# Performance work log

Measured on AMD Instinct MI355X. Metric: run time of the kernel, lower is better.

## Reference

```python
import jax, jax.numpy as jnp
import numpy as np

NUM_HEADS = 16
NEG_INF = float('-inf')


def setup_inputs() -> dict:
    key = jax.random.key(0)
    ks = jax.random.split(key, 8)
    B, S, D = 2, 2048, 1024
    return {
        "query": jax.random.normal(ks[0], (B, S, D), jnp.float32),
        "key": jax.random.normal(ks[1], (B, S, D), jnp.float32),
        "value": jax.random.normal(ks[2], (B, S, D), jnp.float32),
        "attention_mask": jnp.zeros((B, S, S), dtype=bool),
        "Wq": jax.random.normal(ks[3], (D, D), jnp.float32) * (D ** -0.5),
        "Wk": jax.random.normal(ks[4], (D, D), jnp.float32) * (D ** -0.5),
        "Wv": jax.random.normal(ks[5], (D, D), jnp.float32) * (D ** -0.5),
        "Wout": jax.random.normal(ks[6], (D, D), jnp.float32) * (D ** -0.5),
        "b_out": jnp.zeros((D,), jnp.float32),
        "is_causal": 1,
    }


def reference(query, key, value, attention_mask, Wq, Wk, Wv, Wout, b_out, is_causal):
    B, q_len, D = query.shape
    k_len = key.shape[1]
    H = NUM_HEADS
    dk = D // H
    # projections (torch Linear: x @ W.T), split heads -> [B, H, S, dk]
    q = (query @ Wq.T).reshape(B, q_len, H, dk).transpose(0, 2, 1, 3)
    k = (key @ Wk.T).reshape(B, k_len, H, dk).transpose(0, 2, 1, 3)
    v = (value @ Wv.T).reshape(B, k_len, H, dk).transpose(0, 2, 1, 3)
    scores = jnp.einsum('bhqd,bhkd->bhqk', q, k) / jnp.sqrt(jnp.float32(dk))
    if is_causal:
        causal = jnp.triu(jnp.ones((q_len, k_len), dtype=bool), k=1)
        scores = jnp.where(causal, NEG_INF, scores)
    # attn_mask True -> masked out; broadcast over heads
    scores = jnp.where(attention_mask[:, None, :, :], NEG_INF, scores)
    attn = jax.nn.softmax(scores, axis=-1)
    attn = jnp.where(jnp.isnan(attn), 0.0, attn)  # fully-masked rows -> 0
    out = jnp.einsum('bhqk,bhkd->bhqd', attn, v)
    out = out.transpose(0, 2, 1, 3).reshape(B, q_len, D)
    return out @ Wout.T + b_out
```

## Files before the change

kernel.cpp:

```cpp
#include <hip/hip_runtime.h>
#include <hip/hip_bf16.h>

typedef __attribute__((ext_vector_type(8))) short bf16x8;
typedef __attribute__((ext_vector_type(4))) float f32x4;
typedef unsigned long long u64;
typedef unsigned int u32;

#define MFMA(a,b,c) __builtin_amdgcn_mfma_f32_16x16x32_bf16(a,b,c,0,0,0)
#define NEG_INF (-__builtin_inff())
#define SCALE2 0.1803368801111244f

__device__ __forceinline__ unsigned short f2b(float f) {
  unsigned int u = __float_as_uint(f);
  u = u + 0x7fffu + ((u >> 16) & 1u);
  return (unsigned short)(u >> 16);
}

__device__ __forceinline__ u32 pkbf(float lo, float hi) {
  __hip_bfloat162 h = __float22bfloat162_rn(float2{lo, hi});
  return *reinterpret_cast<u32*>(&h);
}

__device__ __forceinline__ void gload_lds16(const unsigned short* g, unsigned short* l) {
  __builtin_amdgcn_global_load_lds((const __attribute__((address_space(1))) void*)g,
                                   (__attribute__((address_space(3))) void*)l, 16, 0, 0);
}

__global__ void cvt7(const float* s0, const float* s1, const float* s2,
                     const float* s3, const float* s4, const float* s5, const float* s6,
                     unsigned short* d0, unsigned short* d1, unsigned short* d2,
                     unsigned short* d3, unsigned short* d4, unsigned short* d5, unsigned short* d6,
                     int nbig, int nsmall) {
  const float* s; unsigned short* d; int n4;
  switch (blockIdx.y) {
    case 0: s=s0; d=d0; n4=nbig; break;
    case 1: s=s1; d=d1; n4=nbig; break;
    case 2: s=s2; d=d2; n4=nbig; break;
    case 3: s=s3; d=d3; n4=nsmall; break;
    case 4: s=s4; d=d4; n4=nsmall; break;
    case 5: s=s5; d=d5; n4=nsmall; break;
    default: s=s6; d=d6; n4=nsmall; break;
  }
  int i = blockIdx.x * blockDim.x + threadIdx.x;
  if (i < n4) {
    float4 v = reinterpret_cast<const float4*>(s)[i];
    ushort4 o;
    o.x = f2b(v.x); o.y = f2b(v.y); o.z = f2b(v.z); o.w = f2b(v.w);
    reinterpret_cast<ushort4*>(d)[i] = o;
  }
}

__global__ void pack_mask(const unsigned char* __restrict__ am, u64* __restrict__ pm, int nU) {
  int lane = threadIdx.x & 63;
  int wid = blockIdx.x * (blockDim.x >> 6) + (threadIdx.x >> 6);
  int stride = gridDim.x * (blockDim.x >> 6);
  for (int u = wid; u < nU; u += stride) {
    unsigned char v = am[(size_t)u * 64 + lane];
    u64 m = __ballot(v != 0);
    if (lane == 0) pm[u] = m;
  }
}

__global__ void mask_summary(const u64* __restrict__ pm, u32* __restrict__ ms, int rows, int nkt) {
  int lane = threadIdx.x & 63;
  int wid = (blockIdx.x * blockDim.x + threadIdx.x) >> 6;
  int nw = (gridDim.x * blockDim.x) >> 6;
  for (int rp = wid; rp < (rows >> 1); rp += nw) {
    int row = rp * 2 + (lane >> 5);
    int t = lane & 31;
    u64 v = pm[(size_t)row * nkt + t];
    u64 bm = __ballot(v != 0ULL);
    if (lane == 0)  ms[rp*2]     = (u32)bm;
    if (lane == 32) ms[rp*2 + 1] = (u32)(bm >> 32);
  }
}

__global__ __launch_bounds__(256) void qkv128s(
    const unsigned short* __restrict__ A,
    const unsigned short* __restrict__ Bw,
    unsigned short* __restrict__ Cqk,
    unsigned short* __restrict__ Cv)
{
  const int K = 1024;
  __shared__ unsigned short As[128*32];
  __shared__ unsigned short Bs[128*32];
  const int tid  = threadIdx.x;
  const int w    = tid >> 6, lane = tid & 63;
  const int wr   = w >> 1,   wc   = w & 1;
  const int g    = lane >> 4, li  = lane & 15;
  const int m0   = blockIdx.x * 128, n0 = blockIdx.y * 128;
  const int bq0  = (m0 >> 12) * 1024 + n0;

  f32x4 acc[4][4] = {};

  const int rS0 = (w*2+0)*16 + (lane>>2);
  const int rS1 = (w*2+1)*16 + (lane>>2);
  const int cS  = (lane&3)*8;
  const unsigned short* gA0 = A  + (size_t)(m0+rS0)*K + cS;
  const unsigned short* gA1 = A  + (size_t)(m0+rS1)*K + cS;
  const unsigned short* gB0 = Bw + (size_t)(bq0+rS0)*K + cS;
  const unsigned short* gB1 = Bw + (size_t)(bq0+rS1)*K + cS;
  unsigned short* lA0 = &As[(w*2+0)*512];
  unsigned short* lA1 = &As[(w*2+1)*512];
  unsigned short* lB0 = &Bs[(w*2+0)*512];
  unsigned short* lB1 = &Bs[(w*2+1)*512];

  for (int k0 = 0; k0 < K; k0 += 32) {
    gload_lds16(gA0 + k0, lA0);
    gload_lds16(gA1 + k0, lA1);
    gload_lds16(gB0 + k0, lB0);
    gload_lds16(gB1 + k0, lB1);
    __syncthreads();

    bf16x8 af[4], bf[4];
    #pragma unroll
    for (int i = 0; i < 4; ++i)
      af[i] = *(const bf16x8*)(&As[(wr*64 + i*16 + li)*32 + g*8]);
    #pragma unroll
    for (int j = 0; j < 4; ++j)
      bf[j] = *(const bf16x8*)(&Bs[(wc*64 + j*16 + li)*32 + g*8]);
    #pragma unroll
    for (int i = 0; i < 4; ++i)
      #pragma unroll
      for (int j = 0; j < 4; ++j)
        acc[i][j] = MFMA(af[i], bf[j], acc[i][j]);
    __syncthreads();
  }

  #pragma unroll
  for (int i = 0; i < 4; ++i) {
    #pragma unroll
    for (int j = 0; j < 4; ++j) {
      int col = n0 + wc*64 + j*16 + li;
      #pragma unroll
      for (int r = 0; r < 4; ++r) {
        int row = m0 + wr*64 + i*16 + g*4 + r;
        float v = acc[i][j][r];
        if (row < 8192) {
          size_t addr = (((size_t)(row >> 11) * 16 + (col >> 6)) * 2048 + (row & 2047)) * 64 + (col & 63);
          Cqk[addr] = f2b(v);
        } else {
          int tk = row & 4095;
          size_t addr = (((size_t)(tk >> 11) * 16 + (col >> 6)) * 64 + (col & 63)) * 2048 + (tk & 2047);
          Cv[addr] = f2b(v);
        }
      }
    }
  }
}

__global__ __launch_bounds__(256) void gemm64x64(
    const unsigned short* __restrict__ A,
    const unsigned short* __restrict__ Bw,
    float* __restrict__ Cf,
    const float* __restrict__ bias,
    int M, int N, int K)
{
  const int NT = 32;
  __shared__ unsigned short As[2][64*32];
  __shared__ unsigned short Bs[2][64*32];
  const int tid  = threadIdx.x;
  const int w    = tid >> 6, lane = tid & 63;
  const int wr   = w >> 1,   wc   = w & 1;
  const int g    = lane >> 4, li  = lane & 15;
  const int m0   = blockIdx.x * 64, n0 = blockIdx.y * 64;

  f32x4 acc[2][2] = {};
  const int crow = lane >> 2, ccol = (lane & 3) * 8;
  const unsigned short* gA = A  + (size_t)(m0 + w*16 + crow)*K + ccol;
  const unsigned short* gB = Bw + (size_t)(n0 + w*16 + crow)*K + ccol;

  gload_lds16(gA, &As[0][w*512]);
  gload_lds16(gB, &Bs[0][w*512]);
  __syncthreads();

  for (int t = 0; t < NT; ++t) {
    const int cur = t & 1;
    if (t + 1 < NT) {
      const int k1 = (t + 1) * 32;
      gload_lds16(gA + k1, &As[cur^1][w*512]);
      gload_lds16(gB + k1, &Bs[cur^1][w*512]);
    }
    bf16x8 af[2], bf[2];
    #pragma unroll
    for (int i = 0; i < 2; ++i)
      af[i] = *(const bf16x8*)(&As[cur][(wr*32 + i*16 + li)*32 + g*8]);
    #pragma unroll
    for (int j = 0; j < 2; ++j)
      bf[j] = *(const bf16x8*)(&Bs[cur][(wc*32 + j*16 + li)*32 + g*8]);
    #pragma unroll
    for (int i = 0; i < 2; ++i)
      #pragma unroll
      for (int j = 0; j < 2; ++j)
        acc[i][j] = MFMA(af[i], bf[j], acc[i][j]);
    __syncthreads();
  }

  #pragma unroll
  for (int i = 0; i < 2; ++i) {
    #pragma unroll
    for (int j = 0; j < 2; ++j) {
      int col = n0 + wc*32 + j*16 + li;
      #pragma unroll
      for (int r = 0; r < 4; ++r) {
        int row = m0 + wr*32 + i*16 + g*4 + r;
        Cf[(size_t)row*N + col] = acc[i][j][r] + bias[col];
      }
    }
  }
}

__global__ __launch_bounds__(256, 4) void attn_kernel(
    const unsigned short* __restrict__ Qh,
    const unsigned short* __restrict__ Kh,
    const unsigned short* __restrict__ Vt,
    const u64* __restrict__ pmask,
    const u32* __restrict__ msum,
    const int* __restrict__ causal_p,
    unsigned short* __restrict__ Ob,
    int B, int H, int S)
{
  __shared__ unsigned short Ks [64*64];
  __shared__ unsigned short Vts[64*64];

  const int tid = threadIdx.x, w = tid >> 6, lane = tid & 63;
  const int g = lane >> 4, li = lane & 15;
  const int nkt = S >> 6, nqt = S >> 6;
  const int causal = causal_p[0];

  int id = blockIdx.x;
  int par = (id ^ (id >> 8)) & 1;
  int qh  = ((id >> 1) & 15) ^ (((id >> 8) & 3) << 2);
  int bh  = id >> 5;
  int qt  = par ? (nqt - 1 - qh) : qh;
  const int q0 = qt << 6;
  const int b = bh / H, h = bh % H;
  const size_t baseK = (size_t)bh * S * 64;
  const size_t baseV = (size_t)bh * 64 * S;

  const int qg = q0 + w*16 + li;
  const unsigned short* qp = Qh + baseK + (size_t)qg*64 + g*8;
  const bf16x8 qf0 = *(const bf16x8*)(qp);
  const bf16x8 qf1 = *(const bf16x8*)(qp + 32);

  const u32 sOr = msum[(size_t)b*S + qg];

  f32x4 oacc[4] = {};
  float mrun = -1e30f, lrun = 0.f;

  const int colk  = (lane & 7) ^ ((lane >> 3) & 7);
  const int ldrow = lane >> 3;
  const int ntile = causal ? (qt + 1) : nkt;

  for (int t = 0; t < ntile; ++t) {
    const int kv0 = t << 6;
    __syncthreads();
    #pragma unroll
    for (int s2 = 0; s2 < 2; ++s2) {
      int u = w*2 + s2;
      gload_lds16(Kh + baseK + (size_t)(kv0 + u*8 + ldrow)*64 + colk*8, &Ks[u*512]);
      gload_lds16(Vt + baseV + (size_t)(u*8 + ldrow)*S + kv0 + colk*8, &Vts[u*512]);
    }
    __syncthreads();

    f32x4 sa[4];
    #pragma unroll
    for (int ni = 0; ni < 4; ++ni) sa[ni] = (f32x4){0.f, 0.f, 0.f, 0.f};
    #pragma unroll
    for (int ni = 0; ni < 4; ++ni) {
      int row = ni*16 + li, rx = row & 7;
      bf16x8 k0 = *(const bf16x8*)(&Ks[row*64 + ((g     ^ rx))*8]);
      bf16x8 k1 = *(const bf16x8*)(&Ks[row*64 + (((4+g) ^ rx))*8]);
      sa[ni] = MFMA(k0, qf0, sa[ni]);
      sa[ni] = MFMA(k1, qf1, sa[ni]);
    }

    const bool edge   = (causal != 0) && (t == ntile - 1);
    const bool doMask = __any(((sOr >> t) & 1u) != 0u);
    float corr = 1.0f;
    bool rescale = true;

    if (!edge && !doMask) {
      float pe[4][4];
      #pragma unroll
      for (int ni = 0; ni < 4; ++ni)
        #pragma unroll
        for (int r = 0; r < 4; ++r)
          pe[ni][r] = exp2f(fmaf(sa[ni][r], SCALE2, -mrun));
      float a0 = fmaxf(sa[0][0], sa[0][1]), a1 = fmaxf(sa[0][2], sa[0][3]);
      float a2 = fmaxf(sa[1][0], sa[1][1]), a3 = fmaxf(sa[1][2], sa[1][3]);
      float a4 = fmaxf(sa[2][0], sa[2][1]), a5 = fmaxf(sa[2][2], sa[2][3]);
      float a6 = fmaxf(sa[3][0], sa[3][1]), a7 = fmaxf(sa[3][2], sa[3][3]);
      float mx = fmaxf(fmaxf(fmaxf(a0,a1), fmaxf(a2,a3)),
                       fmaxf(fmaxf(a4,a5), fmaxf(a6,a7)));
      mx = fmaxf(mx, __shfl_xor(mx, 16));
      mx = fmaxf(mx, __shfl_xor(mx, 32));
      float mxs = mx * SCALE2;
      if (__all(mxs <= mrun + 8.0f)) {
        float s0 = (pe[0][0]+pe[0][1]) + (pe[0][2]+pe[0][3]);
        float s1 = (pe[1][0]+pe[1][1]) + (pe[1][2]+pe[1][3]);
        float s2 = (pe[2][0]+pe[2][1]) + (pe[2][2]+pe[2][3]);
        float s3 = (pe[3][0]+pe[3][1]) + (pe[3][2]+pe[3][3]);
        float rs = (s0+s1) + (s2+s3);
        rs += __shfl_xor(rs, 16);
        rs += __shfl_xor(rs, 32);
        lrun += rs;
        #pragma unroll
        for (int ni = 0; ni < 4; ++ni)
          #pragma unroll
          for (int r = 0; r < 4; ++r)
            sa[ni][r] = pe[ni][r];
        rescale = false;
      } else {
        float mu = fmaxf(mrun, mxs);
        corr = exp2f(mrun - mu);
        float rs = 0.f;
        #pragma unroll
        for (int ni = 0; ni < 4; ++ni)
          #pragma unroll
          for (int r = 0; r < 4; ++r) {
            float p = exp2f(fmaf(sa[ni][r], SCALE2, -mu));
            sa[ni][r] = p;
            rs += p;
          }
        rs += __shfl_xor(rs, 16);
        rs += __shfl_xor(rs, 32);
        lrun = lrun * corr + rs;
        mrun = mu;
      }
    } else {
      u64 mrow = doMask ? pmask[((size_t)b*S + qg) * nkt + t] : 0ULL;
      #pragma unroll
      for (int ni = 0; ni < 4; ++ni)
        #pragma unroll
        for (int r = 0; r < 4; ++r) {
          int kvloc = ni*16 + g*4 + r;
          bool dead = (edge && (kv0 + kvloc > qg)) || ((mrow >> kvloc) & 1ULL);
          sa[ni][r] = dead ? NEG_INF : sa[ni][r] * SCALE2;
        }
      float mx = sa[0][0];
      #pragma unroll
      for (int ni = 0; ni < 4; ++ni)
        #pragma unroll
        for (int r = 0; r < 4; ++r)
          if (ni + r) mx = fmaxf(mx, sa[ni][r]);
      mx = fmaxf(mx, __shfl_xor(mx, 16));
      mx = fmaxf(mx, __shfl_xor(mx, 32));
      float mu = fmaxf(mrun, mx);
      corr = exp2f(mrun - mu);
      float rs = 0.f;
      #pragma unroll
      for (int ni = 0; ni < 4; ++ni)
        #pragma unroll
        for (int r = 0; r < 4; ++r) {
          float pe = exp2f(sa[ni][r] - mu);
          sa[ni][r] = pe;
          rs += pe;
        }
      rs += __shfl_xor(rs, 16);
      rs += __shfl_xor(rs, 32);
      lrun = lrun * corr + rs;
      mrun = mu;
    }

    bf16x8 pf[2];
    #pragma unroll
    for (int c = 0; c < 2; ++c) {
      u32 PA0 = pkbf(sa[2*c  ][0], sa[2*c  ][1]);
      u32 PA1 = pkbf(sa[2*c  ][2], sa[2*c  ][3]);
      u32 PB0 = pkbf(sa[2*c+1][0], sa[2*c+1][1]);
      u32 PB1 = pkbf(sa[2*c+1][2], sa[2*c+1][3]);
      u32 X16_0 = (u32)__shfl_xor((int)((g==2) ? PB0 : PA0), 16);
      u32 X16_1 = (u32)__shfl_xor((int)((g==2) ? PB1 : PA1), 16);
      u32 X32_0 = (u32)__shfl_xor((int)((g==0) ? PB0 : PA0), 32);
      u32 X32_1 = (u32)__shfl_xor((int)((g==0) ? PB1 : PA1), 32);
      u32 X48_0 = (u32)__shfl_xor((int)((g==1) ? PB0 : PA0), 48);
      u32 X48_1 = (u32)__shfl_xor((int)((g==1) ? PB1 : PA1), 48);
      union { u32 u[4]; bf16x8 v; } pbu;
      pbu.u[0] = (g==0) ? PA0   : (g==1) ? X48_0 : (g==2) ? X32_0 : X16_0;
      pbu.u[1] = (g==0) ? PA1   : (g==1) ? X48_1 : (g==2) ? X32_1 : X16_1;
      pbu.u[2] = (g==0) ? X16_0 : (g==1) ? X32_0 : (g==2) ? X48_0 : PB0;
      pbu.u[3] = (g==0) ? X16_1 : (g==1) ? X32_1 : (g==2) ? X48_1 : PB1;
      pf[c] = pbu.v;
    }

    if (rescale) {
      #pragma unroll
      for (int di = 0; di < 4; ++di) {
        oacc[di][0] *= corr; oacc[di][1] *= corr;
        oacc[di][2] *= corr; oacc[di][3] *= corr;
      }
    }

    #pragma unroll
    for (int c = 0; c < 2; ++c) {
      #pragma unroll
      for (int di = 0; di < 4; ++di) {
        int d = di*16 + li;
        bf16x8 vf = *(const bf16x8*)(&Vts[d*64 + (((c*4+g) ^ (d&7)))*8]);
        oacc[di] = MFMA(vf, pf[c], oacc[di]);
      }
    }
  }

  __syncthreads();
  unsigned short* scr = &Ks[w*1024];
  float rl = (lrun > 0.f) ? 1.0f / lrun : 0.f;
  #pragma unroll
  for (int di = 0; di < 4; ++di)
    #pragma unroll
    for (int r = 0; r < 4; ++r) {
      int d = di*16 + g*4 + r;
      scr[li*64 + (((d>>3) ^ (li&7)))*8 + (d&7)] = f2b(oacc[di][r] * rl);
    }
  const int D = H * 64;
  #pragma unroll
  for (int rr = 0; rr < 2; ++rr) {
    int q = rr*8 + (lane >> 3);
    int sl = lane & 7;
    bf16x8 v = *(const bf16x8*)(&scr[q*64 + ((sl ^ (q & 7)))*8]);
    *(bf16x8*)(Ob + (size_t)(b*S + q0 + w*16 + q)*D + h*64 + sl*8) = v;
  }
}

extern "C" void kernel_launch(void* const* d_in, const int* in_sizes, int n_in,
                              void* d_out, int out_size, void* d_ws, size_t ws_size,
                              hipStream_t stream) {
  const float* query = (const float*)d_in[0];
  const float* key_  = (const float*)d_in[1];
  const float* value = (const float*)d_in[2];
  const unsigned char* amask = (const unsigned char*)d_in[3];
  const float* Wq   = (const float*)d_in[4];
  const float* Wk   = (const float*)d_in[5];
  const float* Wv   = (const float*)d_in[6];
  const float* Wout = (const float*)d_in[7];
  const float* b_out = (const float*)d_in[8];
  const int* is_causal = (const int*)d_in[9];
  float* out = (float*)d_out;

  const int B = 2, S = 2048, D = 1024, H = 16;
  const int M = B * S;
  const size_t nx = (size_t)M * D;
  const size_t nw = (size_t)D * D;
  const int nU = B * S * (S / 64);

  unsigned short* ws = (unsigned short*)d_ws;
  unsigned short* xq = ws;
  unsigned short* xk = xq + nx;
  unsigned short* xv = xk + nx;
  unsigned short* wq = xv + nx;
  unsigned short* wk = wq + nw;
  unsigned short* wv = wk + nw;
  unsigned short* wo = wv + nw;
  unsigned short* qb = wo + nw;
  unsigned short* kb = qb + nx;
  unsigned short* vt = kb + nx;
  u32* msum = (u32*)(vt + nx);
  unsigned short* ob = xq;
  u64* pmask = (u64*)xv;

  cvt7<<<dim3((unsigned)(nx/4/256), 7), 256, 0, stream>>>(
      query, key_, value, Wq, Wk, Wv, Wout,
      xq, xk, xv, wq, wk, wv, wo, (int)(nx/4), (int)(nw/4));

  qkv128s<<<dim3(3*M/128, D/128), 256, 0, stream>>>(xq, wq, qb, vt);

  pack_mask<<<512, 256, 0, stream>>>(amask, pmask, nU);
  mask_summary<<<128, 256, 0, stream>>>(pmask, msum, M, S/64);

  attn_kernel<<<dim3((S/64) * B * H), 256, 0, stream>>>(qb, kb, vt, pmask, msum, is_causal, ob, B, H, S);

  gemm64x64<<<dim3(M/64, D/64), 256, 0, stream>>>(ob, wo, out, b_out, M, D, D);
}
```

Baseline: 168.0 us.

## Balance causal attention work by splitting long query tiles across two blocks

In the causal case, each block now handles one short query tile fully plus the first part of a long tile's KV range, and a second set of blocks handles the remainder of the long tiles. The partial outputs are written in bf16 with per-row max and sum, then merged by a new combine kernel. The goal is an equal 16-tile workload per block and less tail imbalance from the triangular work. In exchange it adds a kernel launch, extra global traffic for the partials, and a second bf16 rounding of those partial outputs.

```diff
diff --git a/kernel.cpp b/kernel.cpp
--- a/kernel.cpp
+++ b/kernel.cpp
@@ -14,6 +14,11 @@
   unsigned int u = __float_as_uint(f);
   u = u + 0x7fffu + ((u >> 16) & 1u);
   return (unsigned short)(u >> 16);
+}
+
+__device__ __forceinline__ float b2f(unsigned short s) {
+  unsigned int u = ((unsigned int)s) << 16;
+  return __uint_as_float(u);
 }
 
 __device__ __forceinline__ u32 pkbf(float lo, float hi) {
@@ -210,6 +215,151 @@
   }
 }
 
+__device__ __forceinline__ void attn_tile(
+    const unsigned short* __restrict__ Ks, const unsigned short* __restrict__ Vts,
+    const bf16x8& qf0, const bf16x8& qf1,
+    float& mrun, float& lrun, f32x4* oacc,
+    bool edge, bool doMask, const u64* __restrict__ prow,
+    int t, int kv0, int qg, int g, int li)
+{
+  f32x4 sa[4];
+  #pragma unroll
+  for (int ni = 0; ni < 4; ++ni) sa[ni] = (f32x4){0.f, 0.f, 0.f, 0.f};
+  #pragma unroll
+  for (int ni = 0; ni < 4; ++ni) {
+    int row = ni*16 + li, rx = row & 7;
+    bf16x8 k0 = *(const bf16x8*)(&Ks[row*64 + ((g     ^ rx))*8]);
+    bf16x8 k1 = *(const bf16x8*)(&Ks[row*64 + (((4+g) ^ rx))*8]);
+    sa[ni] = MFMA(k0, qf0, sa[ni]);
+    sa[ni] = MFMA(k1, qf1, sa[ni]);
+  }
+
+  float corr = 1.0f;
+  bool rescale = true;
+
+  if (!edge && !doMask) {
+    float pe[4][4];
+    #pragma unroll
+    for (int ni = 0; ni < 4; ++ni)
+      #pragma unroll
+      for (int r = 0; r < 4; ++r)
+        pe[ni][r] = exp2f(fmaf(sa[ni][r], SCALE2, -mrun));
+    float a0 = fmaxf(sa[0][0], sa[0][1]), a1 = fmaxf(sa[0][2], sa[0][3]);
+    float a2 = fmaxf(sa[1][0], sa[1][1]), a3 = fmaxf(sa[1][2], sa[1][3]);
+    float a4 = fmaxf(sa[2][0], sa[2][1]), a5 = fmaxf(sa[2][2], sa[2][3]);
+    float a6 = fmaxf(sa[3][0], sa[3][1]), a7 = fmaxf(sa[3][2], sa[3][3]);
+    float mx = fmaxf(fmaxf(fmaxf(a0,a1), fmaxf(a2,a3)),
+                     fmaxf(fmaxf(a4,a5), fmaxf(a6,a7)));
+    mx = fmaxf(mx, __shfl_xor(mx, 16));
+    mx = fmaxf(mx, __shfl_xor(mx, 32));
+    float mxs = mx * SCALE2;
+    if (__all(mxs <= mrun + 8.0f)) {
+      float s0 = (pe[0][0]+pe[0][1]) + (pe[0][2]+pe[0][3]);
+      float s1 = (pe[1][0]+pe[1][1]) + (pe[1][2]+pe[1][3]);
+      float s2 = (pe[2][0]+pe[2][1]) + (pe[2][2]+pe[2][3]);
+      float s3 = (pe[3][0]+pe[3][1]) + (pe[3][2]+pe[3][3]);
+      float rs = (s0+s1) + (s2+s3);
+      rs += __shfl_xor(rs, 16);
+      rs += __shfl_xor(rs, 32);
+      lrun += rs;
+      #pragma unroll
+      for (int ni = 0; ni < 4; ++ni)
+        #pragma unroll
+        for (int r = 0; r < 4; ++r)
+          sa[ni][r] = pe[ni][r];
+      rescale = false;
+    } else {
+      float mu = fmaxf(mrun, mxs);
+      corr = exp2f(mrun - mu);
+      float rs = 0.f;
+      #pragma unroll
+      for (int ni = 0; ni < 4; ++ni)
+        #pragma unroll
+        for (int r = 0; r < 4; ++r) {
+          float p = exp2f(fmaf(sa[ni][r], SCALE2, -mu));
+          sa[ni][r] = p;
+          rs += p;
+        }
+      rs += __shfl_xor(rs, 16);
+      rs += __shfl_xor(rs, 32);
+      lrun = lrun * corr + rs;
+      mrun = mu;
+    }
+  } else {
+    u64 mrow = doMask ? prow[t] : 0ULL;
+    #pragma unroll
+    for (int ni = 0; ni < 4; ++ni)
+      #pragma unroll
+      for (int r = 0; r < 4; ++r) {
+        int kvloc = ni*16 + g*4 + r;
+        bool dead = (edge && (kv0 + kvloc > qg)) || ((mrow >> kvloc) & 1ULL);
+        sa[ni][r] = dead ? NEG_INF : sa[ni][r] * SCALE2;
+      }
+    float mx = sa[0][0];
+    #pragma unroll
+    for (int ni = 0; ni < 4; ++ni)
+      #pragma unroll
+      for (int r = 0; r < 4; ++r)
+        if (ni + r) mx = fmaxf(mx, sa[ni][r]);
+    mx = fmaxf(mx, __shfl_xor(mx, 16));
+    mx = fmaxf(mx, __shfl_xor(mx, 32));
+    float mu = fmaxf(mrun, mx);
+    corr = exp2f(mrun - mu);
+    float rs = 0.f;
+    #pragma unroll
+    for (int ni = 0; ni < 4; ++ni)
+      #pragma unroll
+      for (int r = 0; r < 4; ++r) {
+        float pe = exp2f(sa[ni][r] - mu);
+        sa[ni][r] = pe;
+        rs += pe;
+      }
+    rs += __shfl_xor(rs, 16);
+    rs += __shfl_xor(rs, 32);
+    lrun = lrun * corr + rs;
+    mrun = mu;
+  }
+
+  bf16x8 pf[2];
+  #pragma unroll
+  for (int c = 0; c < 2; ++c) {
+    u32 PA0 = pkbf(sa[2*c  ][0], sa[2*c  ][1]);
+    u32 PA1 = pkbf(sa[2*c  ][2], sa[2*c  ][3]);
+    u32 PB0 = pkbf(sa[2*c+1][0], sa[2*c+1][1]);
+    u32 PB1 = pkbf(sa[2*c+1][2], sa[2*c+1][3]);
+    u32 X16_0 = (u32)__shfl_xor((int)((g==2) ? PB0 : PA0), 16);
+    u32 X16_1 = (u32)__shfl_xor((int)((g==2) ? PB1 : PA1), 16);
+    u32 X32_0 = (u32)__shfl_xor((int)((g==0) ? PB0 : PA0), 32);
+    u32 X32_1 = (u32)__shfl_xor((int)((g==0) ? PB1 : PA1), 32);
+    u32 X48_0 = (u32)__shfl_xor((int)((g==1) ? PB0 : PA0), 48);
+    u32 X48_1 = (u32)__shfl_xor((int)((g==1) ? PB1 : PA1), 48);
+    union { u32 u[4]; bf16x8 v; } pbu;
+    pbu.u[0] = (g==0) ? PA0   : (g==1) ? X48_0 : (g==2) ? X32_0 : X16_0;
+    pbu.u[1] = (g==0) ? PA1   : (g==1) ? X48_1 : (g==2) ? X32_1 : X16_1;
+    pbu.u[2] = (g==0) ? X16_0 : (g==1) ? X32_0 : (g==2) ? X48_0 : PB0;
+    pbu.u[3] = (g==0) ? X16_1 : (g==1) ? X32_1 : (g==2) ? X48_1 : PB1;
+    pf[c] = pbu.v;
+  }
+
+  if (rescale) {
+    #pragma unroll
+    for (int di = 0; di < 4; ++di) {
+      oacc[di][0] *= corr; oacc[di][1] *= corr;
+      oacc[di][2] *= corr; oacc[di][3] *= corr;
+    }
+  }
+
+  #pragma unroll
+  for (int c = 0; c < 2; ++c) {
+    #pragma unroll
+    for (int di = 0; di < 4; ++di) {
+      int d = di*16 + li;
+      bf16x8 vf = *(const bf16x8*)(&Vts[d*64 + (((c*4+g) ^ (d&7)))*8]);
+      oacc[di] = MFMA(vf, pf[c], oacc[di]);
+    }
+  }
+}
+
 __global__ __launch_bounds__(256, 4) void attn_kernel(
     const unsigned short* __restrict__ Qh,
     const unsigned short* __restrict__ Kh,
@@ -218,6 +368,9 @@
     const u32* __restrict__ msum,
     const int* __restrict__ causal_p,
     unsigned short* __restrict__ Ob,
+    unsigned short* __restrict__ Opart,
+    float* __restrict__ Mp,
+    float* __restrict__ Lp,
     int B, int H, int S)
 {
   __shared__ unsigned short Ks [64*64];
@@ -225,202 +378,216 @@
 
   const int tid = threadIdx.x, w = tid >> 6, lane = tid & 63;
   const int g = lane >> 4, li = lane & 15;
-  const int nkt = S >> 6, nqt = S >> 6;
+  const int nkt = S >> 6;
   const int causal = causal_p[0];
 
-  int id = blockIdx.x;
-  int par = (id ^ (id >> 8)) & 1;
-  int qh  = ((id >> 1) & 15) ^ (((id >> 8) & 3) << 2);
-  int bh  = id >> 5;
-  int qt  = par ? (nqt - 1 - qh) : qh;
-  const int q0 = qt << 6;
-  const int b = bh / H, h = bh % H;
+  const int id = blockIdx.x;
+  const int bh = id & 31;
+  const int j  = id >> 5;
+  const int b = bh >> 4, h = bh & 15;
   const size_t baseK = (size_t)bh * S * 64;
   const size_t baseV = (size_t)bh * 64 * S;
-
-  const int qg = q0 + w*16 + li;
-  const unsigned short* qp = Qh + baseK + (size_t)qg*64 + g*8;
-  const bf16x8 qf0 = *(const bf16x8*)(qp);
-  const bf16x8 qf1 = *(const bf16x8*)(qp + 32);
-
-  const u32 sOr = msum[(size_t)b*S + qg];
-
-  f32x4 oacc[4] = {};
-  float mrun = -1e30f, lrun = 0.f;
-
   const int colk  = (lane & 7) ^ ((lane >> 3) & 7);
   const int ldrow = lane >> 3;
-  const int ntile = causal ? (qt + 1) : nkt;
-
-  for (int t = 0; t < ntile; ++t) {
-    const int kv0 = t << 6;
+  const int D = H * 64;
+
+  if (!causal) {
+    const int q0 = j << 6;
+    const int qg = q0 + w*16 + li;
+    const unsigned short* qp = Qh + baseK + (size_t)qg*64 + g*8;
+    const bf16x8 qf0 = *(const bf16x8*)(qp);
+    const bf16x8 qf1 = *(const bf16x8*)(qp + 32);
+    const u32 sOr = msum[(size_t)b*S + qg];
+    const u64* prow = pmask + (size_t)(b*S + qg) * nkt;
+    f32x4 oacc[4] = {};
+    float mrun = -1e30f, lrun = 0.f;
+    for (int t = 0; t < nkt; ++t) {
+      const int kv0 = t << 6;
+      __syncthreads();
+      #pragma unroll
+      for (int s2 = 0; s2 < 2; ++s2) {
+        int u = w*2 + s2;
+        gload_lds16(Kh + baseK + (size_t)(kv0 + u*8 + ldrow)*64 + colk*8, &Ks[u*512]);
+        gload_lds16(Vt + baseV + (size_t)(u*8 + ldrow)*S + kv0 + colk*8, &Vts[u*512]);
+      }
+      __syncthreads();
+      const bool doMask = __any(((sOr >> t) & 1u) != 0u);
+      attn_tile(Ks, Vts, qf0, qf1, mrun, lrun, oacc, false, doMask, prow, t, kv0, qg, g, li);
+    }
     __syncthreads();
-    #pragma unroll
-    for (int s2 = 0; s2 < 2; ++s2) {
-      int u = w*2 + s2;
-      gload_lds16(Kh + baseK + (size_t)(kv0 + u*8 + ldrow)*64 + colk*8, &Ks[u*512]);
-      gload_lds16(Vt + baseV + (size_t)(u*8 + ldrow)*S + kv0 + colk*8, &Vts[u*512]);
-    }
-    __syncthreads();
-
-    f32x4 sa[4];
-    #pragma unroll
-    for (int ni = 0; ni < 4; ++ni) sa[ni] = (f32x4){0.f, 0.f, 0.f, 0.f};
-    #pragma unroll
-    for (int ni = 0; ni < 4; ++ni) {
-      int row = ni*16 + li, rx = row & 7;
-      bf16x8 k0 = *(const bf16x8*)(&Ks[row*64 + ((g     ^ rx))*8]);
-      bf16x8 k1 = *(const bf16x8*)(&Ks[row*64 + (((4+g) ^ rx))*8]);
-      sa[ni] = MFMA(k0, qf0, sa[ni]);
-      sa[ni] = MFMA(k1, qf1, sa[ni]);
-    }
-
-    const bool edge   = (causal != 0) && (t == ntile - 1);
-    const bool doMask = __any(((sOr >> t) & 1u) != 0u);
-    float corr = 1.0f;
-    bool rescale = true;
-
-    if (!edge && !doMask) {
-      float pe[4][4];
-      #pragma unroll
-      for (int ni = 0; ni < 4; ++ni)
+    unsigned short* scr = &Ks[w*1024];
+    float rl = (lrun > 0.f) ? 1.0f / lrun : 0.f;
+    #pragma unroll
+    for (int di = 0; di < 4; ++di)
+      #pragma unroll
+      for (int r = 0; r < 4; ++r) {
+        int d = di*16 + g*4 + r;
+        scr[li*64 + (((d>>3) ^ (li&7)))*8 + (d&7)] = f2b(oacc[di][r] * rl);
+      }
+    #pragma unroll
+    for (int rr = 0; rr < 2; ++rr) {
+      int q = rr*8 + (lane >> 3);
+      int sl = lane & 7;
+      bf16x8 v = *(const bf16x8*)(&scr[q*64 + ((sl ^ (q & 7)))*8]);
+      *(bf16x8*)(Ob + (size_t)(b*S + q0 + w*16 + q)*D + h*64 + sl*8) = v;
+    }
+    return;
+  }
+
+  if (j < 16) {
+    {
+      const int qt = j, q0 = qt << 6;
+      const int qg = q0 + w*16 + li;
+      const unsigned short* qp = Qh + baseK + (size_t)qg*64 + g*8;
+      const bf16x8 qf0 = *(const bf16x8*)(qp);
+      const bf16x8 qf1 = *(const bf16x8*)(qp + 32);
+      const u32 sOr = msum[(size_t)b*S + qg];
+      const u64* prow = pmask + (size_t)(b*S + qg) * nkt;
+      f32x4 oacc[4] = {};
+      float mrun = -1e30f, lrun = 0.f;
+      for (int t = 0; t <= qt; ++t) {
+        const int kv0 = t << 6;
+        __syncthreads();
+        #pragma unroll
+        for (int s2 = 0; s2 < 2; ++s2) {
+          int u = w*2 + s2;
+          gload_lds16(Kh + baseK + (size_t)(kv0 + u*8 + ldrow)*64 + colk*8, &Ks[u*512]);
+          gload_lds16(Vt + baseV + (size_t)(u*8 + ldrow)*S + kv0 + colk*8, &Vts[u*512]);
+        }
+        __syncthreads();
+        const bool edge = (t == qt);
+        const bool doMask = __any(((sOr >> t) & 1u) != 0u);
+        attn_tile(Ks, Vts, qf0, qf1, mrun, lrun, oacc, edge, doMask, prow, t, kv0, qg, g, li);
+      }
+      __syncthreads();
+      unsigned short* scr = &Ks[w*1024];
+      float rl = (lrun > 0.f) ? 1.0f / lrun : 0.f;
+      #pragma unroll
+      for (int di = 0; di < 4; ++di)
+        #pragma unroll
+        for (int r = 0; r < 4; ++r) {
+          int d = di*16 + g*4 + r;
+          scr[li*64 + (((d>>3) ^ (li&7)))*8 + (d&7)] = f2b(oacc[di][r] * rl);
+        }
+      #pragma unroll
+      for (int rr = 0; rr < 2; ++rr) {
+        int q = rr*8 + (lane >> 3);
+        int sl = lane & 7;
+        bf16x8 v = *(const bf16x8*)(&scr[q*64 + ((sl ^ (q & 7)))*8]);
+        *(bf16x8*)(Ob + (size_t)(b*S + q0 + w*16 + q)*D + h*64 + sl*8) = v;
+      }
+    }
+    {
+      const int qtH = 31 - j, q0 = qtH << 6;
+      const int qg = q0 + w*16 + li;
+      const unsigned short* qp = Qh + baseK + (size_t)qg*64 + g*8;
+      const bf16x8 qf0 = *(const bf16x8*)(qp);
+      const bf16x8 qf1 = *(const bf16x8*)(qp + 32);
+      const u32 sOr = msum[(size_t)b*S + qg];
+      const u64* prow = pmask + (size_t)(b*S + qg) * nkt;
+      f32x4 oacc[4] = {};
+      float mrun = -1e30f, lrun = 0.f;
+      const int nt2 = 15 - j;
+      for (int t = 0; t < nt2; ++t) {
+        const int kv0 = t << 6;
+        __syncthreads();
+        #pragma unroll
+        for (int s2 = 0; s2 < 2; ++s2) {
+          int u = w*2 + s2;
+          gload_lds16(Kh + baseK + (size_t)(kv0 + u*8 + ldrow)*64 + colk*8, &Ks[u*512]);
+          gload_lds16(Vt + baseV + (size_t)(u*8 + ldrow)*S + kv0 + colk*8, &Vts[u*512]);
+        }
+        __syncthreads();
+        const bool doMask = __any(((sOr >> t) & 1u) != 0u);
+        attn_tile(Ks, Vts, qf0, qf1, mrun, lrun, oacc, false, doMask, prow, t, kv0, qg, g, li);
+      }
+      const int rec = (bh*16 + j)*2 + 0;
+      unsigned short* dst = Opart + (size_t)rec*4096 + (w*64 + lane)*16;
+      #pragma unroll
+      for (int di = 0; di < 4; ++di)
         #pragma unroll
         for (int r = 0; r < 4; ++r)
-          pe[ni][r] = exp2f(fmaf(sa[ni][r], SCALE2, -mrun));
-      float a0 = fmaxf(sa[0][0], sa[0][1]), a1 = fmaxf(sa[0][2], sa[0][3]);
-      float a2 = fmaxf(sa[1][0], sa[1][1]), a3 = fmaxf(sa[1][2], sa[1][3]);
-      float a4 = fmaxf(sa[2][0], sa[2][1]), a5 = fmaxf(sa[2][2], sa[2][3]);
-      float a6 = fmaxf(sa[3][0], sa[3][1]), a7 = fmaxf(sa[3][2], sa[3][3]);
-      float mx = fmaxf(fmaxf(fmaxf(a0,a1), fmaxf(a2,a3)),
-                       fmaxf(fmaxf(a4,a5), fmaxf(a6,a7)));
-      mx = fmaxf(mx, __shfl_xor(mx, 16));
-      mx = fmaxf(mx, __shfl_xor(mx, 32));
-      float mxs = mx * SCALE2;
-      if (__all(mxs <= mrun + 8.0f)) {
-        float s0 = (pe[0][0]+pe[0][1]) + (pe[0][2]+pe[0][3]);
-        float s1 = (pe[1][0]+pe[1][1]) + (pe[1][2]+pe[1][3]);
-        float s2 = (pe[2][0]+pe[2][1]) + (pe[2][2]+pe[2][3]);
-        float s3 = (pe[3][0]+pe[3][1]) + (pe[3][2]+pe[3][3]);
-        float rs = (s0+s1) + (s2+s3);
-        rs += __shfl_xor(rs, 16);
-        rs += __shfl_xor(rs, 32);
-        lrun += rs;
-        #pragma unroll
-        for (int ni = 0; ni < 4; ++ni)
-          #pragma unroll
-          for (int r = 0; r < 4; ++r)
-            sa[ni][r] = pe[ni][r];
-        rescale = false;
-      } else {
-        float mu = fmaxf(mrun, mxs);
-        corr = exp2f(mrun - mu);
-        float rs = 0.f;
-        #pragma unroll
-        for (int ni = 0; ni < 4; ++ni)
-          #pragma unroll
-          for (int r = 0; r < 4; ++r) {
-            float p = exp2f(fmaf(sa[ni][r], SCALE2, -mu));
-            sa[ni][r] = p;
-            rs += p;
-          }
-        rs += __shfl_xor(rs, 16);
-        rs += __shfl_xor(rs, 32);
-        lrun = lrun * corr + rs;
-        mrun = mu;
-      }
-    } else {
-      u64 mrow = doMask ? pmask[((size_t)b*S + qg) * nkt + t] : 0ULL;
-      #pragma unroll
-      for (int ni = 0; ni < 4; ++ni)
-        #pragma unroll
-        for (int r = 0; r < 4; ++r) {
-          int kvloc = ni*16 + g*4 + r;
-          bool dead = (edge && (kv0 + kvloc > qg)) || ((mrow >> kvloc) & 1ULL);
-          sa[ni][r] = dead ? NEG_INF : sa[ni][r] * SCALE2;
-        }
-      float mx = sa[0][0];
-      #pragma unroll
-      for (int ni = 0; ni < 4; ++ni)
-        #pragma unroll
-        for (int r = 0; r < 4; ++r)
-          if (ni + r) mx = fmaxf(mx, sa[ni][r]);
-      mx = fmaxf(mx, __shfl_xor(mx, 16));
-      mx = fmaxf(mx, __shfl_xor(mx, 32));
-      float mu = fmaxf(mrun, mx);
-      corr = exp2f(mrun - mu);
-      float rs = 0.f;
-      #pragma unroll
-      for (int ni = 0; ni < 4; ++ni)
-        #pragma unroll
-        for (int r = 0; r < 4; ++r) {
-          float pe = exp2f(sa[ni][r] - mu);
-          sa[ni][r] = pe;
-          rs += pe;
-        }
-      rs += __shfl_xor(rs, 16);
-      rs += __shfl_xor(rs, 32);
-      lrun = lrun * corr + rs;
-      mrun = mu;
-    }
-
-    bf16x8 pf[2];
-    #pragma unroll
-    for (int c = 0; c < 2; ++c) {
-      u32 PA0 = pkbf(sa[2*c  ][0], sa[2*c  ][1]);
-      u32 PA1 = pkbf(sa[2*c  ][2], sa[2*c  ][3]);
-      u32 PB0 = pkbf(sa[2*c+1][0], sa[2*c+1][1]);
-      u32 PB1 = pkbf(sa[2*c+1][2], sa[2*c+1][3]);
-      u32 X16_0 = (u32)__shfl_xor((int)((g==2) ? PB0 : PA0), 16);
-      u32 X16_1 = (u32)__shfl_xor((int)((g==2) ? PB1 : PA1), 16);
-      u32 X32_0 = (u32)__shfl_xor((int)((g==0) ? PB0 : PA0), 32);
-      u32 X32_1 = (u32)__shfl_xor((int)((g==0) ? PB1 : PA1), 32);
-      u32 X48_0 = (u32)__shfl_xor((int)((g==1) ? PB0 : PA0), 48);
-      u32 X48_1 = (u32)__shfl_xor((int)((g==1) ? PB1 : PA1), 48);
-      union { u32 u[4]; bf16x8 v; } pbu;
-      pbu.u[0] = (g==0) ? PA0   : (g==1) ? X48_0 : (g==2) ? X32_0 : X16_0;
-      pbu.u[1] = (g==0) ? PA1   : (g==1) ? X48_1 : (g==2) ? X32_1 : X16_1;
-      pbu.u[2] = (g==0) ? X16_0 : (g==1) ? X32_0 : (g==2) ? X48_0 : PB0;
-      pbu.u[3] = (g==0) ? X16_1 : (g==1) ? X32_1 : (g==2) ? X48_1 : PB1;
-      pf[c] = pbu.v;
-    }
-
-    if (rescale) {
-      #pragma unroll
-      for (int di = 0; di < 4; ++di) {
-        oacc[di][0] *= corr; oacc[di][1] *= corr;
-        oacc[di][2] *= corr; oacc[di][3] *= corr;
-      }
-    }
-
-    #pragma unroll
-    for (int c = 0; c < 2; ++c) {
-      #pragma unroll
-      for (int di = 0; di < 4; ++di) {
-        int d = di*16 + li;
-        bf16x8 vf = *(const bf16x8*)(&Vts[d*64 + (((c*4+g) ^ (d&7)))*8]);
-        oacc[di] = MFMA(vf, pf[c], oacc[di]);
-      }
-    }
-  }
-
-  __syncthreads();
-  unsigned short* scr = &Ks[w*1024];
-  float rl = (lrun > 0.f) ? 1.0f / lrun : 0.f;
-  #pragma unroll
-  for (int di = 0; di < 4; ++di)
-    #pragma unroll
-    for (int r = 0; r < 4; ++r) {
-      int d = di*16 + g*4 + r;
-      scr[li*64 + (((d>>3) ^ (li&7)))*8 + (d&7)] = f2b(oacc[di][r] * rl);
-    }
+          dst[di*4 + r] = f2b(oacc[di][r]);
+      if (g == 0) { Mp[rec*64 + w*16 + li] = mrun; Lp[rec*64 + w*16 + li] = lrun; }
+    }
+  } else {
+    const int jp = j - 16;
+    const int qtH = 31 - jp, q0 = qtH << 6;
+    const int qg = q0 + w*16 + li;
+    const unsigned short* qp = Qh + baseK + (size_t)qg*64 + g*8;
+    const bf16x8 qf0 = *(const bf16x8*)(qp);
+    const bf16x8 qf1 = *(const bf16x8*)(qp + 32);
+    const u32 sOr = msum[(size_t)b*S + qg];
+    const u64* prow = pmask + (size_t)(b*S + qg) * nkt;
+    f32x4 oacc[4] = {};
+    float mrun = -1e30f, lrun = 0.f;
+    const int t0 = 15 - jp;
+    for (int t = t0; t <= qtH; ++t) {
+      const int kv0 = t << 6;
+      __syncthreads();
+      #pragma unroll
+      for (int s2 = 0; s2 < 2; ++s2) {
+        int u = w*2 + s2;
+        gload_lds16(Kh + baseK + (size_t)(kv0 + u*8 + ldrow)*64 + colk*8, &Ks[u*512]);
+        gload_lds16(Vt + baseV + (size_t)(u*8 + ldrow)*S + kv0 + colk*8, &Vts[u*512]);
+      }
+      __syncthreads();
+      const bool edge = (t == qtH);
+      const bool doMask = __any(((sOr >> t) & 1u) != 0u);
+      attn_tile(Ks, Vts, qf0, qf1, mrun, lrun, oacc, edge, doMask, prow, t, kv0, qg, g, li);
+    }
+    const int rec = (bh*16 + jp)*2 + 1;
+    unsigned short* dst = Opart + (size_t)rec*4096 + (w*64 + lane)*16;
+    #pragma unroll
+    for (int di = 0; di < 4; ++di)
+      #pragma unroll
+      for (int r = 0; r < 4; ++r)
+        dst[di*4 + r] = f2b(oacc[di][r]);
+    if (g == 0) { Mp[rec*64 + w*16 + li] = mrun; Lp[rec*64 + w*16 + li] = lrun; }
+  }
+}
+
+__global__ __launch_bounds__(256) void attn_combine(
+    const unsigned short* __restrict__ Opart,
+    const float* __restrict__ Mp, const float* __restrict__ Lp,
+    const int* __restrict__ causal_p,
+    unsigned short* __restrict__ Ob, int H, int S)
+{
+  if (!causal_p[0]) return;
+  const int blk = blockIdx.x;
+  const int bh = blk >> 4, qp = blk & 15;
+  const int qtH = 31 - qp;
+  const int hidx = bh*16 + qp;
+  const int b = bh >> 4, h = bh & 15;
+  const int tid = threadIdx.x;
+  const int q = tid >> 2;
+  const int dbase = (tid & 3) * 16;
+  const int w = q >> 4, li = q & 15;
   const int D = H * 64;
-  #pragma unroll
-  for (int rr = 0; rr < 2; ++rr) {
-    int q = rr*8 + (lane >> 3);
-    int sl = lane & 7;
-    bf16x8 v = *(const bf16x8*)(&scr[q*64 + ((sl ^ (q & 7)))*8]);
-    *(bf16x8*)(Ob + (size_t)(b*S + q0 + w*16 + q)*D + h*64 + sl*8) = v;
-  }
+
+  const int recA = hidx*2 + 0, recB = hidx*2 + 1;
+  float mA = Mp[recA*64 + q], mB = Mp[recB*64 + q];
+  float lA = Lp[recA*64 + q], lB = Lp[recB*64 + q];
+  float m = fmaxf(mA, mB);
+  float sA = exp2f(mA - m), sB = exp2f(mB - m);
+  float denom = sA*lA + sB*lB;
+  float rden = (denom > 0.f) ? 1.0f/denom : 0.f;
+  sA *= rden; sB *= rden;
+
+  const unsigned short* pA = Opart + (size_t)recA*4096;
+  const unsigned short* pB = Opart + (size_t)recB*4096;
+  unsigned short outv[16];
+  #pragma unroll
+  for (int k = 0; k < 16; ++k) {
+    int d = dbase + k;
+    int di = d >> 4, g2 = (d >> 2) & 3, r = d & 3;
+    int idx = (w*64 + g2*16 + li)*16 + di*4 + r;
+    float o = sA * b2f(pA[idx]) + sB * b2f(pB[idx]);
+    outv[k] = f2b(o);
+  }
+  unsigned short* dst = Ob + (size_t)(b*S + qtH*64 + q)*D + h*64 + dbase;
+  #pragma unroll
+  for (int k = 0; k < 16; ++k) dst[k] = outv[k];
 }
 
 extern "C" void kernel_launch(void* const* d_in, const int* in_sizes, int n_in,
@@ -458,6 +625,9 @@
   u32* msum = (u32*)(vt + nx);
   unsigned short* ob = xq;
   u64* pmask = (u64*)xv;
+  unsigned short* Opart = xk;
+  float* Mp = (float*)wq;
+  float* Lp = Mp + 1024*64;
 
   cvt7<<<dim3((unsigned)(nx/4/256), 7), 256, 0, stream>>>(
       query, key_, value, Wq, Wk, Wv, Wout,
@@ -468,7 +638,9 @@
   pack_mask<<<512, 256, 0, stream>>>(amask, pmask, nU);
   mask_summary<<<128, 256, 0, stream>>>(pmask, msum, M, S/64);
 
-  attn_kernel<<<dim3((S/64) * B * H), 256, 0, stream>>>(qb, kb, vt, pmask, msum, is_causal, ob, B, H, S);
+  attn_kernel<<<dim3(1024), 256, 0, stream>>>(qb, kb, vt, pmask, msum, is_causal,
+                                              ob, Opart, Mp, Lp, B, H, S);
+  attn_combine<<<dim3(512), 256, 0, stream>>>(Opart, Mp, Lp, is_causal, ob, H, S);
 
   gemm64x64<<<dim3(M/64, D/64), 256, 0, stream>>>(ob, wo, out, b_out, M, D, D);
 }
```

Measured after the change: 160.9 us (median of 3 runs). 1.04x faster.
